# Kernel optimization log

Hardware: AMD Instinct MI355X
Metric: run time of the kernel (lower is better)

## Reference

```python
import jax, jax.numpy as jnp
import numpy as np

NHID = 512
NCLS = 250
CHUNK = 200  # words per class (equal class_chunks), vocab = NCLS*CHUNK = 50000
N = 2048     # flattened tokens (batch*seq after masking)


def setup_inputs() -> dict:
    key = jax.random.key(0)
    k1, k2, k3, k4, k5 = jax.random.split(key, 5)
    r = 0.1  # init_weights uniform range
    x = jax.random.normal(k1, (N, NHID), dtype=jnp.float32)
    cls_idx = jax.random.randint(k2, (N,), 0, NCLS, dtype=jnp.int64)
    Wc = jax.random.uniform(k3, (NCLS, NHID), jnp.float32, -r, r)   # cls_decoder.weight
    bc = jnp.zeros((NCLS,), jnp.float32)                             # cls_decoder.bias
    Ww = jax.random.uniform(k4, (NCLS, CHUNK, NHID), jnp.float32, -r, r)  # stacked words_decoders weights
    bw = jnp.zeros((NCLS, CHUNK), jnp.float32)                       # stacked words_decoders biases
    return {"x": x, "Wc": Wc, "bc": bc, "Ww": Ww, "bw": bw, "cls_idx": cls_idx}


def reference(x, Wc, bc, Ww, bw, cls_idx):
    # Class logits for every token: cls_decoder(input)
    p_class = jnp.einsum('nh,ch->nc', x, Wc) + bc          # [N, NCLS]
    # Per-class word decoders: each token goes through the Linear of its class.
    # Equivalent to the dict-based index_select + per-class Linear in the
    # original forward (rows reordered per-token instead of grouped by class).
    Wg = Ww[cls_idx]                                       # [N, CHUNK, NHID] irregular gather
    bg = bw[cls_idx]                                       # [N, CHUNK]
    p_words = jnp.einsum('nkh,nh->nk', Wg, x) + bg         # [N, CHUNK]
    # Concatenate class and within-class logits into one array output.
    return jnp.concatenate([p_class, p_words], axis=1)     # [N, NCLS+CHUNK]
```

## Files before the change

kernel.cpp:

```cpp
#include <hip/hip_runtime.h>

#define NHID   512
#define NCLS   250
#define CHUNK  200
#define NTOK   2048
#define NOUT   450
#define NPANW  13
#define NBLK   250
#define NTHR   512
#define MAXTOK 64

typedef __attribute__((ext_vector_type(8))) short bf16x8;
typedef __attribute__((ext_vector_type(4))) float f32x4;

#define MFMA(a, b, c) __builtin_amdgcn_mfma_f32_16x16x32_bf16((a), (b), (c), 0, 0, 0)

__device__ __forceinline__ unsigned hpack(unsigned a, unsigned b) {
    return __builtin_amdgcn_perm(a, b, 0x07060302u);
}

__device__ __forceinline__ void cvt8(float4 va, float4 vb, bf16x8& h, bf16x8& l) {
    unsigned u0 = __float_as_uint(va.x), u1 = __float_as_uint(va.y);
    unsigned u2 = __float_as_uint(va.z), u3 = __float_as_uint(va.w);
    unsigned u4 = __float_as_uint(vb.x), u5 = __float_as_uint(vb.y);
    unsigned u6 = __float_as_uint(vb.z), u7 = __float_as_uint(vb.w);
    union { unsigned w[4]; bf16x8 v; } H, L;
    H.w[0] = hpack(u1, u0); H.w[1] = hpack(u3, u2);
    H.w[2] = hpack(u5, u4); H.w[3] = hpack(u7, u6);
    float r0 = va.x - __uint_as_float(u0 & 0xffff0000u);
    float r1 = va.y - __uint_as_float(u1 & 0xffff0000u);
    float r2 = va.z - __uint_as_float(u2 & 0xffff0000u);
    float r3 = va.w - __uint_as_float(u3 & 0xffff0000u);
    float r4 = vb.x - __uint_as_float(u4 & 0xffff0000u);
    float r5 = vb.y - __uint_as_float(u5 & 0xffff0000u);
    float r6 = vb.z - __uint_as_float(u6 & 0xffff0000u);
    float r7 = vb.w - __uint_as_float(u7 & 0xffff0000u);
    L.w[0] = hpack(__float_as_uint(r1), __float_as_uint(r0));
    L.w[1] = hpack(__float_as_uint(r3), __float_as_uint(r2));
    L.w[2] = hpack(__float_as_uint(r5), __float_as_uint(r4));
    L.w[3] = hpack(__float_as_uint(r7), __float_as_uint(r6));
    h = H.v; l = L.v;
}

__device__ __forceinline__ void async16(const float* g, float* lds_base) {
    __builtin_amdgcn_global_load_lds(
        (const __attribute__((address_space(1))) unsigned*)g,
        (__attribute__((address_space(3))) unsigned*)lds_base, 16, 0, 0);
}

__device__ __forceinline__ void issue_quarter(const float* wbase, int P, int kq,
                                              float* dst, int lane) {
    #pragma unroll
    for (int i = 0; i < 8; ++i) {
        int j  = 2 * i + (lane >> 5);
        int rj = P * 16 + j; if (rj > CHUNK - 1) rj = CHUNK - 1;
        int sl = (lane & 31) ^ (j & 7);
        async16(wbase + (size_t)rj * NHID + kq * 128 + sl * 4, dst + i * 256);
    }
}

__device__ __forceinline__ void class_unit(int u, int wid, int lane, int n, int q,
                                           const float* __restrict__ x,
                                           const float* __restrict__ Wc,
                                           const float* __restrict__ bc,
                                           float* __restrict__ out) {
    const int mt = u >> 1, hn = u & 1;
    const int g4 = (wid >> 2) & 1, kk = wid & 3;
    const int rC = (hn * 8 + g4 * 4 + kk) * 16 + n;
    const bool rv = rC < NCLS;
    const int  rc = rv ? rC : NCLS - 1;
    const float* ap = x  + (size_t)(mt * 16 + n) * NHID + q * 8;
    const float* bp = Wc + (size_t)rc * NHID + q * 8;
    const float bias = bc[rc];
    f32x4 acc = {0.f, 0.f, 0.f, 0.f};
    float4 qa[2][2], qb[2][2];
    #pragma unroll
    for (int j = 0; j < 2; ++j) {
        qa[j][0] = *(const float4*)(ap + j * 32);
        qa[j][1] = *(const float4*)(ap + j * 32 + 4);
        qb[j][0] = *(const float4*)(bp + j * 32);
        qb[j][1] = *(const float4*)(bp + j * 32 + 4);
    }
    #pragma unroll 2
    for (int s = 0; s < 16; ++s) {
        const int b = s & 1;
        bf16x8 ah, al, bh, bl;
        cvt8(qa[b][0], qa[b][1], ah, al);
        cvt8(qb[b][0], qb[b][1], bh, bl);
        acc = MFMA(ah, bh, acc);
        acc = MFMA(al, bh, acc);
        acc = MFMA(ah, bl, acc);
        if (s + 2 < 16) {
            qa[b][0] = *(const float4*)(ap + (s + 2) * 32);
            qa[b][1] = *(const float4*)(ap + (s + 2) * 32 + 4);
            qb[b][0] = *(const float4*)(bp + (s + 2) * 32);
            qb[b][1] = *(const float4*)(bp + (s + 2) * 32 + 4);
        }
    }
    if (rv) {
        #pragma unroll
        for (int i = 0; i < 4; ++i)
            out[(size_t)(mt * 16 + q * 4 + i) * NOUT + rc] = acc[i] + bias;
    }
}

__global__ __launch_bounds__(NTHR)
void cbd_fused(const float* __restrict__ x,  const float* __restrict__ Wc,
               const float* __restrict__ bc, const float* __restrict__ Ww,
               const float* __restrict__ bw, const int* __restrict__ cls_idx,
               float* __restrict__ out)
{
    __shared__ float ringA[5][2][2048];
    __shared__ float ringB[3][2048];
    __shared__ short Afrag[16384];
    __shared__ int   toktmp[MAXTOK];

    const int tid  = threadIdx.x;
    const int wid  = tid >> 6;
    const int lane = tid & 63;
    const int n    = lane & 15;
    const int q    = lane >> 4;
    const int c    = blockIdx.x;

    int myvals[32];
    #pragma unroll
    for (int it = 0; it < 8; ++it) {
        int4 v = *(const int4*)&cls_idx[it * 256 + lane * 4];
        myvals[it*4+0] = v.x; myvals[it*4+1] = v.y;
        myvals[it*4+2] = v.z; myvals[it*4+3] = v.w;
    }
    int cnt = 0;
    #pragma unroll
    for (int j = 0; j < 32; ++j) {
        int idx  = (j >> 2) * 256 + lane * 4 + (j & 3);
        bool hit = (myvals[j] == c);
        unsigned long long m = __ballot(hit);
        if (hit) {
            int pos = cnt + (int)__popcll(m & ((1ull << lane) - 1ull));
            if (pos < MAXTOK) toktmp[pos] = idx;
        }
        cnt += (int)__popcll(m);
    }
    const int cnt1 = cnt < 16 ? cnt : 16;

    const int p0   = wid;
    const int p1   = 8 + wid;
    const int npan = (wid < 5) ? 2 : 1;

    int tkS[4]; bool msk[4]; float bias0 = 0.f, bias1 = 0.f;
    if (cnt) {
        int mytokA = toktmp[n < cnt1 ? n : cnt1 - 1];
        #pragma unroll
        for (int i = 0; i < 4; ++i) {
            tkS[i] = __shfl(mytokA, q * 4 + i);
            msk[i] = (q * 4 + i) < cnt1;
        }
        { int rr = p0 * 16 + n; if (rr > CHUNK - 1) rr = CHUNK - 1;
          bias0 = bw[c * CHUNK + rr]; }
        if (npan == 2) {
            int rr = p1 * 16 + n; if (rr > CHUNK - 1) rr = CHUNK - 1;
            bias1 = bw[c * CHUNK + rr];
        }
        #pragma unroll
        for (int rep = 0; rep < 2; ++rep) {
            int job = tid * 2 + rep;
            int tok = job >> 6, s = (job >> 2) & 15, qq = job & 3;
            int ti  = toktmp[tok < cnt1 ? tok : cnt1 - 1];
            const float* xp = x + (size_t)ti * NHID + s * 32 + qq * 8;
            float4 a0 = *(const float4*)xp, a1 = *(const float4*)(xp + 4);
            bf16x8 hh, ll; cvt8(a0, a1, hh, ll);
            char* ab = (char*)Afrag + tok * 2048 + s * 128;
            *(bf16x8*)(ab + (((qq * 2    ) ^ (tok & 7)) << 4)) = hh;
            *(bf16x8*)(ab + (((qq * 2 + 1) ^ (tok & 7)) << 4)) = ll;
        }
    }
    __syncthreads();

    if (cnt) {
        const float* wbase = Ww + (size_t)c * CHUNK * NHID;
        float* rb0 = (wid < 5) ? &ringA[wid][0][0] : &ringB[wid - 5][0];
        float* rb1 = (wid < 5) ? &ringA[wid][1][0] : rb0;
        const int depth = (wid < 5) ? 2 : 1;
        const int nQ    = npan * 4;

        issue_quarter(wbase, p0, 0, rb0, lane);
        if (depth == 2) issue_quarter(wbase, p0, 1, rb1, lane);

        f32x4 acc = {0.f, 0.f, 0.f, 0.f};
        for (int iq = 0; iq < nQ; ++iq) {
            if (depth == 2 && iq != nQ - 1)
                asm volatile("s_waitcnt vmcnt(8)" ::: "memory");
            else
                asm volatile("s_waitcnt vmcnt(0)" ::: "memory");

            const int kq = iq & 3;
            const float* qb = (depth == 2 && (iq & 1)) ? rb1 : rb0;
            if (kq == 0) { acc[0]=0.f; acc[1]=0.f; acc[2]=0.f; acc[3]=0.f; }

            #pragma unroll
            for (int t4 = 0; t4 < 4; ++t4) {
                const int s = kq * 4 + t4;
                const char* ab = (const char*)Afrag + n * 2048 + s * 128;
                bf16x8 ah = *(const bf16x8*)(ab + (((q*2    ) ^ (n&7)) << 4));
                bf16x8 al = *(const bf16x8*)(ab + (((q*2 + 1) ^ (n&7)) << 4));
                const float* bp = qb + n * 128 + t4 * 32;
                float4 b0 = *(const float4*)(bp + (((q*2    ) ^ (n&7)) << 2));
                float4 b1 = *(const float4*)(bp + (((q*2 + 1) ^ (n&7)) << 2));
                bf16x8 bh, bl; cvt8(b0, b1, bh, bl);
                acc = MFMA(ah, bh, acc);
                acc = MFMA(al, bh, acc);
                acc = MFMA(ah, bl, acc);
            }

            if (kq == 3) {
                const int   P = (iq >= 4) ? p1 : p0;
                const int   r = P * 16 + n;
                const float biasP = (iq >= 4) ? bias1 : bias0;
                if (r < CHUNK) {
                    #pragma unroll
                    for (int i = 0; i < 4; ++i)
                        if (msk[i])
                            out[(size_t)tkS[i] * NOUT + NCLS + r] = acc[i] + biasP;
                }
            }

            const int nx = iq + depth;
            if (nx < nQ)
                issue_quarter(wbase, (nx >= 4) ? p1 : p0, nx & 3,
                              (depth == 2 && (nx & 1)) ? rb1 : rb0, lane);
        }
    }

    class_unit(c, wid, lane, n, q, x, Wc, bc, out);
    if (c < 6) class_unit(NCLS + c, wid, lane, n, q, x, Wc, bc, out);

    if (cnt > 16) {
        const int cw = cnt < MAXTOK ? cnt : MAXTOK;
        const int ov = cw - 16;
        for (int j = tid; j < ov * CHUNK; j += NTHR) {
            const int g  = j / CHUNK;
            const int rr = j - g * CHUNK;
            const int ti = toktmp[16 + g];
            const float4* wr = (const float4*)(Ww + ((size_t)c * CHUNK + rr) * NHID);
            const float4* xr = (const float4*)(x + (size_t)ti * NHID);
            float s0 = 0.f, s1 = 0.f, s2 = 0.f, s3 = 0.f;
            #pragma unroll 4
            for (int k = 0; k < 128; ++k) {
                float4 a = wr[k], b = xr[k];
                s0 += a.x * b.x; s1 += a.y * b.y;
                s2 += a.z * b.z; s3 += a.w * b.w;
            }
            out[(size_t)ti * NOUT + NCLS + rr] =
                (s0 + s1) + (s2 + s3) + bw[c * CHUNK + rr];
        }
    }
}

extern "C" void kernel_launch(void* const* d_in, const int* in_sizes, int n_in,
                              void* d_out, int out_size, void* d_ws, size_t ws_size,
                              hipStream_t stream) {
    const float* x   = (const float*)d_in[0];
    const float* Wc  = (const float*)d_in[1];
    const float* bc  = (const float*)d_in[2];
    const float* Ww  = (const float*)d_in[3];
    const float* bw  = (const float*)d_in[4];
    const int*   cls = (const int*)d_in[5];
    float* out = (float*)d_out;
    hipLaunchKernelGGL(cbd_fused, dim3(NBLK), dim3(NTHR), 0, stream,
                       x, Wc, bc, Ww, bw, cls, out);
}
```

Before: 190.5 us.

## Split each class across two 256-thread blocks and load weights into registers

The grid doubles to 500 blocks of 256 threads, two per class, each covering about half the 13 output panels. The LDS ring buffers and async global-to-LDS loads are replaced by direct register loads of a whole panel row, and launch bounds request two blocks per CU. The class-logit work is redistributed so each wave runs two class units. This aims for more parallelism and lower LDS use, but loses the explicit load/compute pipelining and adds register pressure from the 32 float4 buffer.

```diff
diff --git a/kernel.cpp b/kernel.cpp
--- a/kernel.cpp
+++ b/kernel.cpp
@@ -5,9 +5,8 @@
 #define CHUNK  200
 #define NTOK   2048
 #define NOUT   450
-#define NPANW  13
-#define NBLK   250
-#define NTHR   512
+#define NBLK   500
+#define NTHR   256
 #define MAXTOK 64
 
 typedef __attribute__((ext_vector_type(8))) short bf16x8;
@@ -42,30 +41,13 @@
     h = H.v; l = L.v;
 }
 
-__device__ __forceinline__ void async16(const float* g, float* lds_base) {
-    __builtin_amdgcn_global_load_lds(
-        (const __attribute__((address_space(1))) unsigned*)g,
-        (__attribute__((address_space(3))) unsigned*)lds_base, 16, 0, 0);
-}
-
-__device__ __forceinline__ void issue_quarter(const float* wbase, int P, int kq,
-                                              float* dst, int lane) {
-    #pragma unroll
-    for (int i = 0; i < 8; ++i) {
-        int j  = 2 * i + (lane >> 5);
-        int rj = P * 16 + j; if (rj > CHUNK - 1) rj = CHUNK - 1;
-        int sl = (lane & 31) ^ (j & 7);
-        async16(wbase + (size_t)rj * NHID + kq * 128 + sl * 4, dst + i * 256);
-    }
-}
-
-__device__ __forceinline__ void class_unit(int u, int wid, int lane, int n, int q,
+__device__ __forceinline__ void class_unit(int u, int w8, int lane, int n, int q,
                                            const float* __restrict__ x,
                                            const float* __restrict__ Wc,
                                            const float* __restrict__ bc,
                                            float* __restrict__ out) {
     const int mt = u >> 1, hn = u & 1;
-    const int g4 = (wid >> 2) & 1, kk = wid & 3;
+    const int g4 = (w8 >> 2) & 1, kk = w8 & 3;
     const int rC = (hn * 8 + g4 * 4 + kk) * 16 + n;
     const bool rv = rC < NCLS;
     const int  rc = rv ? rC : NCLS - 1;
@@ -104,14 +86,12 @@
     }
 }
 
-__global__ __launch_bounds__(NTHR)
+__global__ __launch_bounds__(NTHR, 2)
 void cbd_fused(const float* __restrict__ x,  const float* __restrict__ Wc,
                const float* __restrict__ bc, const float* __restrict__ Ww,
                const float* __restrict__ bw, const int* __restrict__ cls_idx,
                float* __restrict__ out)
 {
-    __shared__ float ringA[5][2][2048];
-    __shared__ float ringB[3][2048];
     __shared__ short Afrag[16384];
     __shared__ int   toktmp[MAXTOK];
 
@@ -120,7 +100,8 @@
     const int lane = tid & 63;
     const int n    = lane & 15;
     const int q    = lane >> 4;
-    const int c    = blockIdx.x;
+    const int c    = blockIdx.x >> 1;
+    const int h    = blockIdx.x & 1;
 
     int myvals[32];
     #pragma unroll
@@ -143,11 +124,7 @@
     }
     const int cnt1 = cnt < 16 ? cnt : 16;
 
-    const int p0   = wid;
-    const int p1   = 8 + wid;
-    const int npan = (wid < 5) ? 2 : 1;
-
-    int tkS[4]; bool msk[4]; float bias0 = 0.f, bias1 = 0.f;
+    int tkS[4]; bool msk[4];
     if (cnt) {
         int mytokA = toktmp[n < cnt1 ? n : cnt1 - 1];
         #pragma unroll
@@ -155,15 +132,9 @@
             tkS[i] = __shfl(mytokA, q * 4 + i);
             msk[i] = (q * 4 + i) < cnt1;
         }
-        { int rr = p0 * 16 + n; if (rr > CHUNK - 1) rr = CHUNK - 1;
-          bias0 = bw[c * CHUNK + rr]; }
-        if (npan == 2) {
-            int rr = p1 * 16 + n; if (rr > CHUNK - 1) rr = CHUNK - 1;
-            bias1 = bw[c * CHUNK + rr];
-        }
         #pragma unroll
-        for (int rep = 0; rep < 2; ++rep) {
-            int job = tid * 2 + rep;
+        for (int rep = 0; rep < 4; ++rep) {
+            int job = rep * 256 + tid;
             int tok = job >> 6, s = (job >> 2) & 15, qq = job & 3;
             int ti  = toktmp[tok < cnt1 ? tok : cnt1 - 1];
             const float* xp = x + (size_t)ti * NHID + s * 32 + qq * 8;
@@ -177,64 +148,54 @@
     __syncthreads();
 
     if (cnt) {
-        const float* wbase = Ww + (size_t)c * CHUNK * NHID;
-        float* rb0 = (wid < 5) ? &ringA[wid][0][0] : &ringB[wid - 5][0];
-        float* rb1 = (wid < 5) ? &ringA[wid][1][0] : rb0;
-        const int depth = (wid < 5) ? 2 : 1;
-        const int nQ    = npan * 4;
-
-        issue_quarter(wbase, p0, 0, rb0, lane);
-        if (depth == 2) issue_quarter(wbase, p0, 1, rb1, lane);
-
-        f32x4 acc = {0.f, 0.f, 0.f, 0.f};
-        for (int iq = 0; iq < nQ; ++iq) {
-            if (depth == 2 && iq != nQ - 1)
-                asm volatile("s_waitcnt vmcnt(8)" ::: "memory");
-            else
-                asm volatile("s_waitcnt vmcnt(0)" ::: "memory");
-
-            const int kq = iq & 3;
-            const float* qb = (depth == 2 && (iq & 1)) ? rb1 : rb0;
-            if (kq == 0) { acc[0]=0.f; acc[1]=0.f; acc[2]=0.f; acc[3]=0.f; }
-
+        const int np = h ? 6 : 7;
+        for (int pp = wid; pp < np; pp += 4) {
+            const int P  = h * 7 + pp;
+            const int r  = P * 16 + n;
+            const int rr = r < CHUNK ? r : CHUNK - 1;
+            const float* wrow = Ww + ((size_t)c * CHUNK + rr) * NHID + q * 8;
+
+            float4 breg[32];
             #pragma unroll
-            for (int t4 = 0; t4 < 4; ++t4) {
-                const int s = kq * 4 + t4;
+            for (int s = 0; s < 16; ++s) {
+                breg[2*s]   = *(const float4*)(wrow + s * 32);
+                breg[2*s+1] = *(const float4*)(wrow + s * 32 + 4);
+            }
+            float bias = bw[c * CHUNK + rr];
+            __builtin_amdgcn_sched_barrier(0);
+
+            f32x4 acc = {0.f, 0.f, 0.f, 0.f};
+            #pragma unroll
+            for (int s = 0; s < 16; ++s) {
                 const char* ab = (const char*)Afrag + n * 2048 + s * 128;
                 bf16x8 ah = *(const bf16x8*)(ab + (((q*2    ) ^ (n&7)) << 4));
                 bf16x8 al = *(const bf16x8*)(ab + (((q*2 + 1) ^ (n&7)) << 4));
-                const float* bp = qb + n * 128 + t4 * 32;
-                float4 b0 = *(const float4*)(bp + (((q*2    ) ^ (n&7)) << 2));
-                float4 b1 = *(const float4*)(bp + (((q*2 + 1) ^ (n&7)) << 2));
-                bf16x8 bh, bl; cvt8(b0, b1, bh, bl);
+                bf16x8 bh, bl; cvt8(breg[2*s], breg[2*s+1], bh, bl);
                 acc = MFMA(ah, bh, acc);
                 acc = MFMA(al, bh, acc);
                 acc = MFMA(ah, bl, acc);
             }
 
-            if (kq == 3) {
-                const int   P = (iq >= 4) ? p1 : p0;
-                const int   r = P * 16 + n;
-                const float biasP = (iq >= 4) ? bias1 : bias0;
-                if (r < CHUNK) {
-                    #pragma unroll
-                    for (int i = 0; i < 4; ++i)
-                        if (msk[i])
-                            out[(size_t)tkS[i] * NOUT + NCLS + r] = acc[i] + biasP;
-                }
-            }
-
-            const int nx = iq + depth;
-            if (nx < nQ)
-                issue_quarter(wbase, (nx >= 4) ? p1 : p0, nx & 3,
-                              (depth == 2 && (nx & 1)) ? rb1 : rb0, lane);
-        }
-    }
-
-    class_unit(c, wid, lane, n, q, x, Wc, bc, out);
-    if (c < 6) class_unit(NCLS + c, wid, lane, n, q, x, Wc, bc, out);
-
-    if (cnt > 16) {
+            if (r < CHUNK) {
+                #pragma unroll
+                for (int i = 0; i < 4; ++i)
+                    if (msk[i])
+                        out[(size_t)tkS[i] * NOUT + NCLS + r] = acc[i] + bias;
+            }
+        }
+    }
+
+    {
+        int unit = -1;
+        if (h == 0)          unit = c;
+        else if (c < 6)      unit = NCLS + c;
+        if (unit >= 0) {
+            class_unit(unit, wid,     lane, n, q, x, Wc, bc, out);
+            class_unit(unit, 4 + wid, lane, n, q, x, Wc, bc, out);
+        }
+    }
+
+    if (h == 0 && cnt > 16) {
         const int cw = cnt < MAXTOK ? cnt : MAXTOK;
         const int ov = cw - 16;
         for (int j = tid; j < ov * CHUNK; j += NTHR) {
```

After: 206.8 us. +8.6%, slower.
